# Kernel tuning notes

Hardware: AMD Instinct MI355X
Metric: run time of the kernel (lower is better)

Reference implementation:

```python
import jax, jax.numpy as jnp
import numpy as np

INPUT_DIM, QK_DIM, V_DIM = 1024, 512, 512

def setup_inputs() -> dict:
    key = jax.random.key(0)
    ks = jax.random.split(key, 7)
    B, S = 4, 2048
    scale = 1.0 / np.sqrt(INPUT_DIM)
    return {
        "x": jax.random.normal(ks[0], (B, S, INPUT_DIM), dtype=jnp.float32),
        "Wq": jax.random.normal(ks[1], (INPUT_DIM, QK_DIM), dtype=jnp.float32) * scale,
        "bq": jax.random.normal(ks[2], (QK_DIM,), dtype=jnp.float32) * 0.01,
        "Wk": jax.random.normal(ks[3], (INPUT_DIM, QK_DIM), dtype=jnp.float32) * scale,
        "bk": jax.random.normal(ks[4], (QK_DIM,), dtype=jnp.float32) * 0.01,
        "Wv": jax.random.normal(ks[5], (INPUT_DIM, V_DIM), dtype=jnp.float32) * scale,
        "bv": jax.random.normal(ks[6], (V_DIM,), dtype=jnp.float32) * 0.01,
    }

def reference(x, Wq, bq, Wk, bk, Wv, bv):
    # q,k: (B,S,Dqk), v: (B,S,Dv)
    q = jnp.einsum("bsi,id->bsd", x, Wq) + bq
    k = jnp.einsum("bsi,id->bsd", x, Wk) + bk
    v = jnp.einsum("bsi,id->bsd", x, Wv) + bv
    scale = 1.0 / jnp.sqrt(jnp.asarray(q.shape[-1], q.dtype))
    scores = jnp.einsum("bqd,bkd->bqk", q, k) * scale  # (B,S,S)
    attn = jax.nn.softmax(scores, axis=-1)
    return jnp.einsum("bqk,bkd->bqd", attn, v)
```

## Files before the change

### kernel.cpp

```cpp
#include <hip/hip_runtime.h>

typedef __attribute__((ext_vector_type(8))) short short8;
typedef __attribute__((ext_vector_type(4))) float f32x4;

#define S_    2048
#define DI    1024
#define DQK   512
#define DV    512
#define NTOK  8192

#define GLL(gp, lp) __builtin_amdgcn_global_load_lds( \
    (const __attribute__((address_space(1))) unsigned int*)(gp), \
    (__attribute__((address_space(3))) unsigned int*)(lp), 16, 0, 0)

static __device__ __forceinline__ unsigned short f2bf(float f) {
  unsigned int u = __float_as_uint(f);
  u += 0x7fffu + ((u >> 16) & 1u);
  return (unsigned short)(u >> 16);
}

__global__ void conv_all_kernel(const float* __restrict__ x,
                                const float* __restrict__ W0, const float* __restrict__ W1,
                                const float* __restrict__ W2,
                                unsigned short* __restrict__ xb,
                                unsigned short* __restrict__ T0, unsigned short* __restrict__ T1,
                                unsigned short* __restrict__ T2,
                                float* __restrict__ rowsum) {
  int z = blockIdx.z;
  if (z >= 3) {
    int blk = (z - 3) * 512 + blockIdx.y * 16 + blockIdx.x;
    int idx = (blk * 256 + threadIdx.x) * 8;
    const float4* p = (const float4*)(x + idx);
    float4 f0 = p[0], f1 = p[1];
    uint4 o;
    o.x = (unsigned)f2bf(f0.x) | ((unsigned)f2bf(f0.y) << 16);
    o.y = (unsigned)f2bf(f0.z) | ((unsigned)f2bf(f0.w) << 16);
    o.z = (unsigned)f2bf(f1.x) | ((unsigned)f2bf(f1.y) << 16);
    o.w = (unsigned)f2bf(f1.z) | ((unsigned)f2bf(f1.w) << 16);
    *(uint4*)(xb + idx) = o;
    return;
  }
  __shared__ float tile[32][33];
  int mat = z;
  if (mat == 0 && blockIdx.x == 0)
    rowsum[blockIdx.y * 256 + threadIdx.x] = 0.f;
  const float* W = (mat == 0) ? W0 : (mat == 1) ? W1 : W2;
  unsigned short* T = (mat == 0) ? T0 : (mat == 1) ? T1 : T2;
  int n0 = blockIdx.x * 32, k0 = blockIdx.y * 32;
  int c = threadIdx.x & 31, r0 = threadIdx.x >> 5;
  for (int i = 0; i < 4; ++i) {
    int kk = r0 + i * 8;
    tile[kk][c] = W[(k0 + kk) * DQK + n0 + c];
  }
  __syncthreads();
  for (int i = 0; i < 4; ++i) {
    int nn = r0 + i * 8;
    T[(n0 + nn) * DI + k0 + c] = f2bf(tile[c][nn]);
  }
}

template<int NSTAGE>
__device__ __forceinline__ void gemm_core_128x128(
    const unsigned short* __restrict__ A, const unsigned short* __restrict__ B,
    int lda, int ldb, int K, int m0, int n0,
    unsigned short* As, unsigned short* Bs, f32x4 (&acc)[4][4]) {
  int tid = threadIdx.x, lane = tid & 63, wv = tid >> 6;
  int quad = lane >> 4, l16 = lane & 15;
  int wm = wv >> 1, wn = wv & 1;
  int r0 = wv * 32 + (lane >> 2);
  int c8 = ((lane & 3) ^ ((lane >> 2) & 3)) * 8;
  const unsigned short* ga0 = A + (size_t)(m0 + r0) * lda + c8;
  const unsigned short* ga1 = ga0 + (size_t)16 * lda;
  const unsigned short* gb0 = B + (size_t)(n0 + r0) * ldb + c8;
  const unsigned short* gb1 = gb0 + (size_t)16 * ldb;
  int ldsw0 = (wv * 32) * 32;
  int ldsw1 = ldsw0 + 16 * 32;
#pragma unroll
  for (int i = 0; i < 4; ++i)
#pragma unroll
    for (int j = 0; j < 4; ++j) acc[i][j] = (f32x4){0.f, 0.f, 0.f, 0.f};

  auto stage = [&](int buf, int k0) {
    unsigned short* Ad = As + buf * (128 * 32);
    unsigned short* Bd = Bs + buf * (128 * 32);
    GLL(ga0 + k0, Ad + ldsw0);
    GLL(ga1 + k0, Ad + ldsw1);
    GLL(gb0 + k0, Bd + ldsw0);
    GLL(gb1 + k0, Bd + ldsw1);
  };

  int nk = K >> 5;
  int pc = (quad ^ (l16 & 3)) * 8;
#pragma unroll
  for (int s = 0; s < NSTAGE; ++s) stage(s, s * 32);
  int cur = 0, pre = NSTAGE;
  for (int kt = 0; kt < nk; ++kt) {
    if (kt + NSTAGE <= nk) {
      if constexpr (NSTAGE == 2) { asm volatile("s_waitcnt vmcnt(4)" ::: "memory"); }
      else                       { asm volatile("s_waitcnt vmcnt(12)" ::: "memory"); }
    } else {
      asm volatile("s_waitcnt vmcnt(0)" ::: "memory");
    }
    __builtin_amdgcn_sched_barrier(0);
    __builtin_amdgcn_s_barrier();
    __builtin_amdgcn_sched_barrier(0);
    if (kt + NSTAGE < nk) stage(pre, (kt + NSTAGE) * 32);
    __builtin_amdgcn_sched_barrier(0);
    const unsigned short* Ab = As + cur * (128 * 32);
    const unsigned short* Bb = Bs + cur * (128 * 32);
    short8 af[4], bf[4];
#pragma unroll
    for (int t = 0; t < 4; ++t) {
      af[t] = *(const short8*)(Ab + (wm * 64 + t * 16 + l16) * 32 + pc);
      bf[t] = *(const short8*)(Bb + (wn * 64 + t * 16 + l16) * 32 + pc);
    }
#pragma unroll
    for (int tm = 0; tm < 4; ++tm)
#pragma unroll
      for (int tn = 0; tn < 4; ++tn)
        acc[tm][tn] = __builtin_amdgcn_mfma_f32_16x16x32_bf16(af[tm], bf[tn], acc[tm][tn], 0, 0, 0);
    cur = (cur == NSTAGE) ? 0 : cur + 1;
    pre = (pre == NSTAGE) ? 0 : pre + 1;
  }
}

__global__ __launch_bounds__(256, 2) void qkv_dma_kernel(
    const unsigned short* __restrict__ xb,
    const unsigned short* __restrict__ wqt, const unsigned short* __restrict__ wkt,
    const unsigned short* __restrict__ wvt,
    const float* __restrict__ bq, const float* __restrict__ bk, const float* __restrict__ bv,
    unsigned short* __restrict__ qo, unsigned short* __restrict__ ko,
    unsigned short* __restrict__ vto) {
  __shared__ unsigned short As[3 * 128 * 32];
  __shared__ unsigned short Bs[3 * 128 * 32];
  int bidx = blockIdx.x;
  int xcd = bidx & 7;
  int local = bidx >> 3;
  int mlocal = local & 7;
  int col12 = local >> 3;
  int mat = col12 >> 2;
  int m0 = (xcd * 8 + mlocal) * 128;
  int n0 = (col12 & 3) * 128;
  const unsigned short* wt = (mat == 0) ? wqt : (mat == 1) ? wkt : wvt;
  const float* bias = (mat == 0) ? bq : (mat == 1) ? bk : bv;
  float oscale = (mat == 0) ? 0.04419417382415922f : 1.0f;
  f32x4 acc[4][4];
  gemm_core_128x128<2>(xb, wt, DI, DI, DI, m0, n0, As, Bs, acc);

  int tid = threadIdx.x, lane = tid & 63, wv = tid >> 6;
  int quad = lane >> 4, l16 = lane & 15;
  int wm = wv >> 1, wn = wv & 1;
  bool transp = (mat == 2);
  unsigned short* outp = (mat == 0) ? qo : (mat == 1) ? ko : vto;
#pragma unroll
  for (int tn = 0; tn < 4; ++tn) {
    int col = n0 + wn * 64 + tn * 16 + l16;
    float bc = bias[col];
#pragma unroll
    for (int tm = 0; tm < 4; ++tm) {
      int rowb = m0 + wm * 64 + tm * 16 + quad * 4;
      f32x4 a = acc[tm][tn];
      if (!transp) {
        outp[(size_t)(rowb + 0) * DQK + col] = f2bf((a.x + bc) * oscale);
        outp[(size_t)(rowb + 1) * DQK + col] = f2bf((a.y + bc) * oscale);
        outp[(size_t)(rowb + 2) * DQK + col] = f2bf((a.z + bc) * oscale);
        outp[(size_t)(rowb + 3) * DQK + col] = f2bf((a.w + bc) * oscale);
      } else {
        ushort4 pk;
        pk.x = f2bf(a.x + bc); pk.y = f2bf(a.y + bc);
        pk.z = f2bf(a.z + bc); pk.w = f2bf(a.w + bc);
        *(ushort4*)(outp + (size_t)col * NTOK + rowb) = pk;
      }
    }
  }
}

__global__ __launch_bounds__(256, 2) void s_exp_kernel(
    const unsigned short* __restrict__ q, const unsigned short* __restrict__ k,
    unsigned short* __restrict__ sp, float* __restrict__ rowsum) {
  __shared__ unsigned short As[3 * 128 * 32];
  __shared__ unsigned short Bs[3 * 128 * 32];
  int bidx = blockIdx.x;
  int xcd = bidx & 7, b = xcd >> 1;
  int sub = ((bidx >> 3) << 1) | (xcd & 1);
  int m0 = (sub >> 4) * 128, n0 = (sub & 15) * 128;
  f32x4 acc[4][4];
  gemm_core_128x128<2>(k + (size_t)b * S_ * DQK, q + (size_t)b * S_ * DQK,
                       DQK, DQK, DQK, m0, n0, As, Bs, acc);

  int tid = threadIdx.x, lane = tid & 63, wv = tid >> 6;
  int quad = lane >> 4, l16 = lane & 15;
  int wm = wv >> 1, wn = wv & 1;
  unsigned short* Cb = sp + (size_t)b * S_ * S_;
#pragma unroll
  for (int tn = 0; tn < 4; ++tn) {
    int qrow = n0 + wn * 64 + tn * 16 + l16;
    float rs = 0.f;
#pragma unroll
    for (int tm = 0; tm < 4; ++tm) {
      int kcol = m0 + wm * 64 + tm * 16 + quad * 4;
      f32x4 a = acc[tm][tn];
      float e0 = __expf(a.x), e1 = __expf(a.y), e2 = __expf(a.z), e3 = __expf(a.w);
      ushort4 pk;
      pk.x = f2bf(e0); pk.y = f2bf(e1); pk.z = f2bf(e2); pk.w = f2bf(e3);
      *(ushort4*)(Cb + (size_t)qrow * S_ + kcol) = pk;
      rs += (e0 + e1) + (e2 + e3);
    }
    rs += __shfl_xor(rs, 16);
    rs += __shfl_xor(rs, 32);
    if (quad == 0) atomicAdd(rowsum + b * S_ + qrow, rs);
  }
}

__global__ __launch_bounds__(256, 1) void pv_kernel(
    const unsigned short* __restrict__ sp, const unsigned short* __restrict__ vt,
    const float* __restrict__ rowsum, float* __restrict__ out) {
  __shared__ unsigned short As[5 * 128 * 32];
  __shared__ unsigned short Bs[5 * 128 * 32];
  int bidx = blockIdx.x;
  int xcd = bidx & 7, b = xcd >> 1;
  int local = bidx >> 3;
  int m0 = (((xcd & 1) << 3) | (local >> 2)) * 128;
  int n0 = (local & 3) * 128;
  f32x4 acc[4][4];
  gemm_core_128x128<4>(sp + (size_t)b * S_ * S_, vt + (size_t)b * S_,
                       S_, NTOK, S_, m0, n0, As, Bs, acc);

  int tid = threadIdx.x, lane = tid & 63, wv = tid >> 6;
  int quad = lane >> 4, l16 = lane & 15;
  int wm = wv >> 1, wn = wv & 1;
  float* ob = out + (size_t)b * S_ * DV;
#pragma unroll
  for (int tm = 0; tm < 4; ++tm) {
    int rowb = m0 + wm * 64 + tm * 16 + quad * 4;
    float inv[4];
#pragma unroll
    for (int i = 0; i < 4; ++i) inv[i] = 1.0f / rowsum[b * S_ + rowb + i];
#pragma unroll
    for (int tn = 0; tn < 4; ++tn) {
      int col = n0 + wn * 64 + tn * 16 + l16;
      f32x4 a = acc[tm][tn];
      ob[(size_t)(rowb + 0) * DV + col] = a.x * inv[0];
      ob[(size_t)(rowb + 1) * DV + col] = a.y * inv[1];
      ob[(size_t)(rowb + 2) * DV + col] = a.z * inv[2];
      ob[(size_t)(rowb + 3) * DV + col] = a.w * inv[3];
    }
  }
}

extern "C" void kernel_launch(void* const* d_in, const int* in_sizes, int n_in,
                              void* d_out, int out_size, void* d_ws, size_t ws_size,
                              hipStream_t stream) {
  const float* x  = (const float*)d_in[0];
  const float* Wq = (const float*)d_in[1];
  const float* bq = (const float*)d_in[2];
  const float* Wk = (const float*)d_in[3];
  const float* bk = (const float*)d_in[4];
  const float* Wv = (const float*)d_in[5];
  const float* bv = (const float*)d_in[6];
  float* out = (float*)d_out;

  char* ws = (char*)d_ws;
  unsigned short* xb  = (unsigned short*)(ws);
  unsigned short* wqt = (unsigned short*)(ws + 16777216);
  unsigned short* wkt = (unsigned short*)(ws + 16777216 + 1048576);
  unsigned short* wvt = (unsigned short*)(ws + 16777216 + 2097152);
  unsigned short* qo  = (unsigned short*)(ws + 19922944);
  unsigned short* ko  = (unsigned short*)(ws + 19922944 + 8388608);
  unsigned short* vto = (unsigned short*)(ws + 19922944 + 16777216);
  unsigned short* sp  = (unsigned short*)(ws + 45088768);
  float* rowsum       = (float*)(ws + 45088768 + 33554432);

  dim3 gc(16, 32, 11);
  conv_all_kernel<<<gc, 256, 0, stream>>>(x, Wq, Wk, Wv, xb, wqt, wkt, wvt, rowsum);
  qkv_dma_kernel<<<768, 256, 0, stream>>>(xb, wqt, wkt, wvt, bq, bk, bv, qo, ko, vto);
  s_exp_kernel<<<1024, 256, 0, stream>>>(qo, ko, sp, rowsum);
  pv_kernel<<<256, 256, 0, stream>>>(sp, vto, rowsum, out);
}
```

Baseline: 195.5 us.

## Enlarge QK^T tile to 256x256 with 512 threads; shrink PV pipeline depth

The score kernel moves from 128x128 tiles with 256 threads to 256x256 tiles with 512 threads (8 waves), each wave computing a 128x64 sub-tile. It uses an inline double-buffered global-to-LDS loop with swizzled addressing. The larger tile is meant to cut global/L2 reloads of Q and K and give more MFMA work per LDS fetch. PV kernel pipeline depth drops from 4 to 2 stages to fit two blocks per CU, though its launch grid stays at 256 blocks, so the extra occupancy may not be used. The risks are more register pressure from 32 accumulators per thread and only 256 blocks for the score stage.

Result: no change. 192.5 us (-1.5%).

```diff
diff --git a/kernel.cpp b/kernel.cpp
--- a/kernel.cpp
+++ b/kernel.cpp
@@ -175,30 +175,74 @@
   }
 }
 
-__global__ __launch_bounds__(256, 2) void s_exp_kernel(
+__global__ __launch_bounds__(512, 1) void s_exp_kernel(
     const unsigned short* __restrict__ q, const unsigned short* __restrict__ k,
     unsigned short* __restrict__ sp, float* __restrict__ rowsum) {
-  __shared__ unsigned short As[3 * 128 * 32];
-  __shared__ unsigned short Bs[3 * 128 * 32];
+  __shared__ unsigned short As[2 * 256 * 32];
+  __shared__ unsigned short Bs[2 * 256 * 32];
   int bidx = blockIdx.x;
-  int xcd = bidx & 7, b = xcd >> 1;
-  int sub = ((bidx >> 3) << 1) | (xcd & 1);
-  int m0 = (sub >> 4) * 128, n0 = (sub & 15) * 128;
-  f32x4 acc[4][4];
-  gemm_core_128x128<2>(k + (size_t)b * S_ * DQK, q + (size_t)b * S_ * DQK,
-                       DQK, DQK, DQK, m0, n0, As, Bs, acc);
+  int xcd = bidx & 7, b = xcd >> 1, p = xcd & 1;
+  int local = bidx >> 3;
+  int m0 = (p * 4 + (local & 3)) * 256;
+  int n0 = (local >> 2) * 256;
+  const unsigned short* A = k + (size_t)b * S_ * DQK;
+  const unsigned short* B = q + (size_t)b * S_ * DQK;
 
   int tid = threadIdx.x, lane = tid & 63, wv = tid >> 6;
   int quad = lane >> 4, l16 = lane & 15;
-  int wm = wv >> 1, wn = wv & 1;
+  int wm = wv >> 2, wn = wv & 3;
+  int r0 = wv * 32 + (lane >> 2);
+  int c8 = ((lane & 3) ^ ((lane >> 2) & 3)) * 8;
+  const unsigned short* ga0 = A + (size_t)(m0 + r0) * DQK + c8;
+  const unsigned short* ga1 = ga0 + (size_t)16 * DQK;
+  const unsigned short* gb0 = B + (size_t)(n0 + r0) * DQK + c8;
+  const unsigned short* gb1 = gb0 + (size_t)16 * DQK;
+  int ldsw0 = (wv * 32) * 32;
+  int ldsw1 = ldsw0 + 16 * 32;
+
+  f32x4 acc[8][4];
+#pragma unroll
+  for (int i = 0; i < 8; ++i)
+#pragma unroll
+    for (int j = 0; j < 4; ++j) acc[i][j] = (f32x4){0.f, 0.f, 0.f, 0.f};
+
+  auto stage = [&](int buf, int k0) {
+    GLL(ga0 + k0, As + buf * 8192 + ldsw0);
+    GLL(ga1 + k0, As + buf * 8192 + ldsw1);
+    GLL(gb0 + k0, Bs + buf * 8192 + ldsw0);
+    GLL(gb1 + k0, Bs + buf * 8192 + ldsw1);
+  };
+
+  int pc = (quad ^ (l16 & 3)) * 8;
+  stage(0, 0);
+  for (int kt = 0; kt < 16; ++kt) {
+    int cur = kt & 1;
+    __syncthreads();
+    if (kt + 1 < 16) stage(cur ^ 1, (kt + 1) * 32);
+    const unsigned short* Ab = As + cur * 8192;
+    const unsigned short* Bb = Bs + cur * 8192;
+    short8 af[8], bf[4];
+#pragma unroll
+    for (int t = 0; t < 8; ++t)
+      af[t] = *(const short8*)(Ab + (wm * 128 + t * 16 + l16) * 32 + pc);
+#pragma unroll
+    for (int t = 0; t < 4; ++t)
+      bf[t] = *(const short8*)(Bb + (wn * 64 + t * 16 + l16) * 32 + pc);
+#pragma unroll
+    for (int tm = 0; tm < 8; ++tm)
+#pragma unroll
+      for (int tn = 0; tn < 4; ++tn)
+        acc[tm][tn] = __builtin_amdgcn_mfma_f32_16x16x32_bf16(af[tm], bf[tn], acc[tm][tn], 0, 0, 0);
+  }
+
   unsigned short* Cb = sp + (size_t)b * S_ * S_;
 #pragma unroll
   for (int tn = 0; tn < 4; ++tn) {
     int qrow = n0 + wn * 64 + tn * 16 + l16;
     float rs = 0.f;
 #pragma unroll
-    for (int tm = 0; tm < 4; ++tm) {
-      int kcol = m0 + wm * 64 + tm * 16 + quad * 4;
+    for (int tm = 0; tm < 8; ++tm) {
+      int kcol = m0 + wm * 128 + tm * 16 + quad * 4;
       f32x4 a = acc[tm][tn];
       float e0 = __expf(a.x), e1 = __expf(a.y), e2 = __expf(a.z), e3 = __expf(a.w);
       ushort4 pk;
@@ -212,18 +256,18 @@
   }
 }
 
-__global__ __launch_bounds__(256, 1) void pv_kernel(
+__global__ __launch_bounds__(256, 2) void pv_kernel(
     const unsigned short* __restrict__ sp, const unsigned short* __restrict__ vt,
     const float* __restrict__ rowsum, float* __restrict__ out) {
-  __shared__ unsigned short As[5 * 128 * 32];
-  __shared__ unsigned short Bs[5 * 128 * 32];
+  __shared__ unsigned short As[3 * 128 * 32];
+  __shared__ unsigned short Bs[3 * 128 * 32];
   int bidx = blockIdx.x;
   int xcd = bidx & 7, b = xcd >> 1;
   int local = bidx >> 3;
   int m0 = (((xcd & 1) << 3) | (local >> 2)) * 128;
   int n0 = (local & 3) * 128;
   f32x4 acc[4][4];
-  gemm_core_128x128<4>(sp + (size_t)b * S_ * S_, vt + (size_t)b * S_,
+  gemm_core_128x128<2>(sp + (size_t)b * S_ * S_, vt + (size_t)b * S_,
                        S_, NTOK, S_, m0, n0, As, Bs, acc);
 
   int tid = threadIdx.x, lane = tid & 63, wv = tid >> 6;
@@ -274,6 +318,6 @@
   dim3 gc(16, 32, 11);
   conv_all_kernel<<<gc, 256, 0, stream>>>(x, Wq, Wk, Wv, xb, wqt, wkt, wvt, rowsum);
   qkv_dma_kernel<<<768, 256, 0, stream>>>(xb, wqt, wkt, wvt, bq, bk, bv, qo, ko, vto);
-  s_exp_kernel<<<1024, 256, 0, stream>>>(qo, ko, sp, rowsum);
+  s_exp_kernel<<<256, 512, 0, stream>>>(qo, ko, sp, rowsum);
   pv_kernel<<<256, 256, 0, stream>>>(sp, vto, rowsum, out);
 }
```
